# Performance work log

Hardware: AMD Instinct MI355X
Metric: run time of the kernel (lower is better)

## Reference

```python
import jax, jax.numpy as jnp
import numpy as np

N_HEAD = 12
MIN_SIZE = 4
MAX_SIZE = 8
TOP_M = 16
ALPHA = 1.0
EPS = 1e-6
NEG_INF = -1e30


def setup_inputs() -> dict:
    key = jax.random.key(0)
    ks = jax.random.split(key, 4)
    B, T, C = 2, 512, 768
    x = jax.random.normal(ks[0], (B, T, C), jnp.float32)
    w_qkv = jax.random.normal(ks[1], (C, 3 * C), jnp.float32) * (1.0 / np.sqrt(C))
    b_qkv = jnp.zeros((3 * C,), jnp.float32)
    w_proj = jax.random.normal(ks[2], (C, C), jnp.float32) * (1.0 / np.sqrt(C))
    b_proj = jnp.zeros((C,), jnp.float32)
    gate_param = jnp.zeros((), jnp.float32)  # dpp_gate_init = 0.0 -> gate = 0.5
    return {"x": x, "w_qkv": w_qkv, "b_qkv": b_qkv, "w_proj": w_proj,
            "b_proj": b_proj, "gate_param": gate_param}


def _dpp_token(i, q_i, k, v):
    """Greedy DPP subset selection + attention for one query token.
    q_i: [hd], k/v: [T, hd]. Faithful to the torch greedy loop, vectorized
    over candidates with incremental Gram construction (scores only gate the
    discrete selection, so they are computed under stop_gradient, matching
    torch where they only feed Python comparisons)."""
    T, hd = k.shape
    kc = jax.lax.stop_gradient(k)
    qc = jax.lax.stop_gradient(q_i)
    # causal similarity, topk candidates
    sim = jnp.where(jnp.arange(T) <= i, kc @ qc, NEG_INF)
    _, topidx = jax.lax.top_k(sim, TOP_M)  # [M]
    # candidates = top-min(TOP_M, i+1) causal neighbors, excluding i itself
    cand_active = (jnp.arange(TOP_M) < jnp.minimum(TOP_M, i + 1)) & (topidx != i)
    cand_keys = kc[topidx]                              # [M, hd]
    cnorm = jnp.sum(cand_keys * cand_keys, axis=-1)     # [M]

    sel_idx = jnp.zeros((MAX_SIZE,), jnp.int32).at[0].set(i)
    sel_count = jnp.int32(1)
    # initial score: log(det([k_i.k_i]) + eps) / 1**alpha
    cur = jnp.log(jnp.dot(kc[i], kc[i]) + EPS)
    stopped = jnp.bool_(False)
    eye = jnp.eye(MAX_SIZE, dtype=jnp.float32)
    slots = jnp.arange(MAX_SIZE)

    for _ in range(MAX_SIZE - 1):
        rowmask = slots < sel_count                       # [S] current subset rows
        pos = (slots == sel_count).astype(jnp.float32)    # slot for new candidate
        Ksel = kc[sel_idx] * rowmask[:, None].astype(jnp.float32)  # [S, hd]
        G0 = Ksel @ Ksel.T                                # [S, S]
        cross = cand_keys @ Ksel.T                        # [M, S]
        # Gc[c,a,b] = G0[a,b] + pos[a]*cross[c,b] + pos[b]*cross[c,a] + pos[a]pos[b]*cnorm[c]
        Gc = (G0[None]
              + pos[None, :, None] * cross[:, None, :]
              + pos[None, None, :] * cross[:, :, None]
              + (pos[:, None] * pos[None, :])[None] * cnorm[:, None, None])
        newmask = rowmask | (slots == sel_count)
        # identity-pad unused rows/cols so det equals det of the active submatrix
        Gc = Gc + (eye * (1.0 - newmask.astype(jnp.float32)))[None]
        dets = jnp.linalg.det(Gc)                         # [M] (float32, as torch)
        size = (sel_count + 1).astype(jnp.float32)
        score = jnp.log(dets + EPS) / size ** ALPHA       # minimize_det=False
        masked = jnp.where(cand_active, score, NEG_INF)
        best = jnp.argmax(masked)
        best_score = masked[best]
        any_cand = jnp.any(cand_active)
        take = any_cand & (~stopped) & ((best_score > cur) | (sel_count < MIN_SIZE))
        sel_idx = jnp.where(take, sel_idx.at[sel_count].set(topidx[best].astype(jnp.int32)), sel_idx)
        cand_active = jnp.where(take, cand_active.at[best].set(False), cand_active)
        cur = jnp.where(take, best_score, cur)
        sel_count = sel_count + take.astype(jnp.int32)
        stopped = stopped | (~take)

    # attention over the selected subset (gradients flow through k, v, q here)
    rowmask = slots < sel_count
    Ks = k[sel_idx]
    Vs = v[sel_idx]
    logits = jnp.where(rowmask, (Ks @ q_i) / np.float32(np.sqrt(hd)), NEG_INF)
    w = jax.nn.softmax(logits)
    return w @ Vs


def _forward(x, w_qkv, b_qkv, w_proj, b_proj, gate_param):
    B, T, C = x.shape
    hd = C // N_HEAD
    qkv = x @ w_qkv + b_qkv
    q, k, v = jnp.split(qkv, 3, axis=-1)

    def heads(t):  # [B,T,C] -> [B*NH, T, hd]
        return t.reshape(B, T, N_HEAD, hd).transpose(0, 2, 1, 3).reshape(B * N_HEAD, T, hd)

    q, k, v = heads(q), heads(k), heads(v)

    # standard causal softmax attention (flash path, dropout=0 at eval)
    scale = np.float32(1.0 / np.sqrt(hd))
    att = jnp.einsum('nqd,nkd->nqk', q, k) * scale
    causal = jnp.tril(jnp.ones((T, T), bool))
    att = jnp.where(causal[None], att, NEG_INF)
    y_std = jnp.einsum('nqk,nkd->nqd', jax.nn.softmax(att, axis=-1), v)

    # DPP greedy-selection attention, vmapped over tokens and (batch*head)
    dpp_head = jax.vmap(_dpp_token, in_axes=(0, 0, None, None))
    y_dpp = jax.vmap(lambda qh, kh, vh: dpp_head(jnp.arange(T), qh, kh, vh))(q, k, v)

    gate = jax.nn.sigmoid(gate_param)
    y = gate * y_dpp + (1.0 - gate) * y_std
    y = y.reshape(B, N_HEAD, T, hd).transpose(0, 2, 1, 3).reshape(B, T, C)
    return y @ w_proj + b_proj


def reference(x, w_qkv, b_qkv, w_proj, b_proj, gate_param):
    return _forward(x, w_qkv, b_qkv, w_proj, b_proj, gate_param)
```

## Files before the change

### kernel.cpp

```cpp
#include <hip/hip_runtime.h>
#include <math.h>

constexpr int SEQ   = 512;
constexpr int HDIM  = 64;
constexpr int NHEAD = 12;
constexpr int NBATCH = 2;
constexpr int CDIM  = 768;
constexpr int TOPM  = 16;
constexpr int SMAX  = 8;
constexpr float NEGINF = -1e30f;

typedef short bf16x8 __attribute__((ext_vector_type(8)));
typedef float f32x4  __attribute__((ext_vector_type(4)));

__device__ inline void gload_lds16(const void* src, void* lds_base)
{
    __builtin_amdgcn_global_load_lds(
        (const __attribute__((address_space(1))) void*)src,
        (__attribute__((address_space(3))) void*)lds_base, 16, 0, 0);
}

__device__ inline unsigned short f2bf(float f)
{
    unsigned u = __float_as_uint(f);
    return (unsigned short)((u + 0x7FFFu + ((u >> 16) & 1u)) >> 16);
}
__device__ inline float bf2f(unsigned short h)
{
    return __uint_as_float((unsigned)h << 16);
}

__global__ __launch_bounds__(256) void split_x_kernel(
    const float* __restrict__ x, unsigned short* __restrict__ xh,
    unsigned short* __restrict__ xm, unsigned short* __restrict__ xl)
{
    const int idx = (blockIdx.x * 256 + threadIdx.x) * 4;
    float4 v = *(const float4*)(x + idx);
    float vv[4] = {v.x, v.y, v.z, v.w};
    unsigned short h[4], m[4], l[4];
    #pragma unroll
    for (int e = 0; e < 4; ++e) {
        float f = vv[e];
        unsigned short bh = f2bf(f);
        float r1 = f - bf2f(bh);
        unsigned short bm2 = f2bf(r1);
        float r2 = r1 - bf2f(bm2);
        h[e] = bh; m[e] = bm2; l[e] = f2bf(r2);
    }
    *(ushort4*)(xh + idx) = make_ushort4(h[0], h[1], h[2], h[3]);
    *(ushort4*)(xm + idx) = make_ushort4(m[0], m[1], m[2], m[3]);
    *(ushort4*)(xl + idx) = make_ushort4(l[0], l[1], l[2], l[3]);
}

__global__ __launch_bounds__(256) void tsplit_w_kernel(
    const float* __restrict__ w, unsigned short* __restrict__ wh,
    unsigned short* __restrict__ wm, unsigned short* __restrict__ wl)
{
    __shared__ float T[64][65];
    const int c0 = blockIdx.x * 64;
    const int k0 = blockIdx.y * 64;
    const int tid = threadIdx.x;
    #pragma unroll
    for (int i = 0; i < 16; ++i) {
        int idx = tid + i * 256;
        int kk = idx >> 6, cc = idx & 63;
        T[kk][cc] = w[(size_t)(k0 + kk) * (3 * CDIM) + c0 + cc];
    }
    __syncthreads();
    #pragma unroll
    for (int i = 0; i < 16; ++i) {
        int idx = tid + i * 256;
        int col = idx >> 6, kk = idx & 63;
        float f = T[kk][col];
        unsigned short bh = f2bf(f);
        float r1 = f - bf2f(bh);
        unsigned short bm2 = f2bf(r1);
        float r2 = r1 - bf2f(bm2);
        size_t o = (size_t)(c0 + col) * CDIM + k0 + kk;
        wh[o] = bh; wm[o] = bm2; wl[o] = f2bf(r2);
    }
}

__global__ __launch_bounds__(64) void qkv_mfma_kernel(
    const unsigned short* __restrict__ xh, const unsigned short* __restrict__ xm,
    const unsigned short* __restrict__ xl, const unsigned short* __restrict__ wh,
    const unsigned short* __restrict__ wm, const unsigned short* __restrict__ wl,
    const float* __restrict__ bias,
    float* __restrict__ q, float* __restrict__ k, float* __restrict__ v)
{
    __shared__ unsigned short As[3][64 * 32];
    __shared__ unsigned short Bs[3][64 * 32];
    const int bn = blockIdx.x * 64;
    const int bm = blockIdx.y * 64;
    const int tid = threadIdx.x;
    const int lrow = tid & 15;
    const int lk8 = (tid >> 4) << 3;

    f32x4 acc[4][4];
    #pragma unroll
    for (int a = 0; a < 4; ++a)
        #pragma unroll
        for (int b = 0; b < 4; ++b)
            acc[a][b] = (f32x4){0.f, 0.f, 0.f, 0.f};

    const unsigned short* xs[3] = {xh, xm, xl};
    const unsigned short* wsrc[3] = {wh, wm, wl};

    for (int k0 = 0; k0 < CDIM; k0 += 32) {
        #pragma unroll
        for (int c = 0; c < 3; ++c) {
            #pragma unroll
            for (int l = 0; l < 4; ++l) {
                int slot = l * 64 + tid;
                int row = slot >> 2;
                int k8 = (slot & 3) << 3;
                gload_lds16(xs[c] + (size_t)(bm + row) * CDIM + k0 + k8,
                            &As[c][l * 512]);
            }
        }
        #pragma unroll
        for (int c = 0; c < 3; ++c) {
            #pragma unroll
            for (int l = 0; l < 4; ++l) {
                int slot = l * 64 + tid;
                int col = slot >> 2;
                int k8 = (slot & 3) << 3;
                gload_lds16(wsrc[c] + (size_t)(bn + col) * CDIM + k0 + k8,
                            &Bs[c][l * 512]);
            }
        }
        __syncthreads();

        bf16x8 bf[3][4];
        #pragma unroll
        for (int c = 0; c < 3; ++c)
            #pragma unroll
            for (int ni = 0; ni < 4; ++ni)
                bf[c][ni] = *(const bf16x8*)&Bs[c][(ni * 16 + lrow) * 32 + lk8];

        #pragma unroll
        for (int mi = 0; mi < 4; ++mi) {
            bf16x8 ah = *(const bf16x8*)&As[0][(mi * 16 + lrow) * 32 + lk8];
            bf16x8 am = *(const bf16x8*)&As[1][(mi * 16 + lrow) * 32 + lk8];
            bf16x8 al = *(const bf16x8*)&As[2][(mi * 16 + lrow) * 32 + lk8];
            #pragma unroll
            for (int ni = 0; ni < 4; ++ni) {
                f32x4 a = acc[mi][ni];
                a = __builtin_amdgcn_mfma_f32_16x16x32_bf16(al, bf[0][ni], a, 0, 0, 0);
                a = __builtin_amdgcn_mfma_f32_16x16x32_bf16(ah, bf[2][ni], a, 0, 0, 0);
                a = __builtin_amdgcn_mfma_f32_16x16x32_bf16(am, bf[1][ni], a, 0, 0, 0);
                a = __builtin_amdgcn_mfma_f32_16x16x32_bf16(am, bf[0][ni], a, 0, 0, 0);
                a = __builtin_amdgcn_mfma_f32_16x16x32_bf16(ah, bf[1][ni], a, 0, 0, 0);
                a = __builtin_amdgcn_mfma_f32_16x16x32_bf16(ah, bf[0][ni], a, 0, 0, 0);
                acc[mi][ni] = a;
            }
        }
        __syncthreads();
    }

    const int rbase = (tid >> 4) << 2;
    #pragma unroll
    for (int mi = 0; mi < 4; ++mi) {
        #pragma unroll
        for (int ni = 0; ni < 4; ++ni) {
            int cc = bn + ni * 16 + lrow;
            float bval = bias[cc];
            int part = cc / CDIM;
            int c2 = cc - part * CDIM;
            int hh = c2 >> 6, d = c2 & 63;
            float* dst = (part == 0) ? q : ((part == 1) ? k : v);
            #pragma unroll
            for (int r = 0; r < 4; ++r) {
                int m = bm + mi * 16 + rbase + r;
                int b_ = m >> 9, t = m & 511;
                dst[((((size_t)b_ * NHEAD + hh) * SEQ) + t) * HDIM + d] =
                    acc[mi][ni][r] + bval;
            }
        }
    }
}

__global__ __launch_bounds__(256) void qkkt_kernel(
    const float* __restrict__ q, const float* __restrict__ k,
    float* __restrict__ S, float* __restrict__ KKT)
{
    __shared__ float Qs[64][68];
    __shared__ float Ka[64][68];
    __shared__ float Kb[64][68];
    const int e = blockIdx.x;
    const int n = blockIdx.y;
    int it = 0, start = 0;
    while (start + it + 1 <= e) { start += it + 1; ++it; }
    const int jt = e - start;
    const int tid = threadIdx.x;
    const float* qh = q + (size_t)n * SEQ * HDIM;
    const float* kh = k + (size_t)n * SEQ * HDIM;

    #pragma unroll
    for (int l = 0; l < 4; ++l) {
        int idx = tid + l * 256;
        int tok = idx >> 4, d4 = (idx & 15) << 2;
        *(float4*)&Qs[tok][d4] = *(const float4*)(qh + (it * 64 + tok) * HDIM + d4);
        *(float4*)&Ka[tok][d4] = *(const float4*)(kh + (it * 64 + tok) * HDIM + d4);
        *(float4*)&Kb[tok][d4] = *(const float4*)(kh + (jt * 64 + tok) * HDIM + d4);
    }
    __syncthreads();

    const int tm = (tid >> 4) << 2;
    const int tn = (tid & 15) << 2;
    float sacc[4][4] = {};
    float gacc[4][4] = {};
    #pragma unroll 4
    for (int d4 = 0; d4 < 16; ++d4) {
        float4 qr[4], ar[4], br[4];
        #pragma unroll
        for (int u = 0; u < 4; ++u) {
            qr[u] = *(const float4*)&Qs[tm + u][d4 << 2];
            ar[u] = *(const float4*)&Ka[tm + u][d4 << 2];
        }
        #pragma unroll
        for (int w2 = 0; w2 < 4; ++w2)
            br[w2] = *(const float4*)&Kb[tn + w2][d4 << 2];
        #pragma unroll
        for (int u = 0; u < 4; ++u)
            #pragma unroll
            for (int w2 = 0; w2 < 4; ++w2) {
                float s = sacc[u][w2];
                s = fmaf(qr[u].x, br[w2].x, s);
                s = fmaf(qr[u].y, br[w2].y, s);
                s = fmaf(qr[u].z, br[w2].z, s);
                s = fmaf(qr[u].w, br[w2].w, s);
                sacc[u][w2] = s;
                float g = gacc[u][w2];
                g = fmaf(ar[u].x, br[w2].x, g);
                g = fmaf(ar[u].y, br[w2].y, g);
                g = fmaf(ar[u].z, br[w2].z, g);
                g = fmaf(ar[u].w, br[w2].w, g);
                gacc[u][w2] = g;
            }
    }
    float* gdst = KKT + ((size_t)n * 36 + e) * 4096;
    #pragma unroll
    for (int u = 0; u < 4; ++u) {
        int i = it * 64 + tm + u;
        float4 o = {sacc[u][0], sacc[u][1], sacc[u][2], sacc[u][3]};
        *(float4*)(S + ((size_t)n * SEQ + i) * SEQ + jt * 64 + tn) = o;
        float4 g = {gacc[u][0], gacc[u][1], gacc[u][2], gacc[u][3]};
        *(float4*)(gdst + (tm + u) * 64 + tn) = g;
    }
}

__device__ inline double hybrid_log(double a)
{
    unsigned long long b = __double_as_longlong(a);
    int e2 = (int)((b >> 52) & 0x7FF) - 1022;
    double m = __longlong_as_double((b & 0x000FFFFFFFFFFFFFULL) |
                                    0x3FE0000000000000ULL);
    return ((double)__log2f((float)m) + (double)e2) * 0.6931471805599453;
}

__device__ inline double rsqrt64(double x)
{
    double r = (double)rsqrtf((float)x);
    r = r * (1.5 - 0.5 * x * r * r);
    return r;
}

#define CSW(a, b)                                                        \
    {                                                                    \
        bool sw = (v##a < v##b) || ((v##a == v##b) && (j##a > j##b));    \
        float tf = sw ? v##b : v##a;                                     \
        float uf = sw ? v##a : v##b;                                     \
        int ti = sw ? j##b : j##a;                                       \
        int ui = sw ? j##a : j##b;                                       \
        v##a = tf; v##b = uf; j##a = ti; j##b = ui;                      \
    }

__global__ __launch_bounds__(128) void dpp_kernel(
    const float* __restrict__ v, float* __restrict__ S,
    const float* __restrict__ KKT, const float* __restrict__ gate_p,
    float* __restrict__ y, float* __restrict__ denomArr)
{
    const int tid  = threadIdx.x;
    const int wid  = tid >> 6;
    const int lane = tid & 63;
    const int i = blockIdx.x * 2 + wid;
    const int n = blockIdx.y;
    const float* vh = v + (size_t)n * SEQ * HDIM;
    const float* KKTh = KKT + (size_t)n * 36 * 4096;
    float* Srow = S + ((size_t)n * SEQ + i) * SEQ;

    __shared__ float prow[2][SEQ];
    __shared__ float gramf[2][17][17];
    __shared__ int   eidx[2][17];
    __shared__ int   selS[2][SMAX];

    float sim8[8];
    #pragma unroll
    for (int m = 0; m < 8; ++m) {
        int j = lane + (m << 6);
        sim8[m] = (j <= i) ? Srow[j] : NEGINF;
    }
    if (lane < SMAX) selS[wid][lane] = i;

    {
        float v0 = sim8[0], v1 = sim8[1], v2 = sim8[2], v3 = sim8[3],
              v4 = sim8[4], v5 = sim8[5], v6 = sim8[6], v7 = sim8[7];
        int j0 = lane, j1 = lane + 64, j2 = lane + 128, j3 = lane + 192,
            j4 = lane + 256, j5 = lane + 320, j6 = lane + 384, j7 = lane + 448;
        CSW(0, 1) CSW(2, 3) CSW(4, 5) CSW(6, 7)
        CSW(0, 2) CSW(1, 3) CSW(4, 6) CSW(5, 7)
        CSW(1, 2) CSW(5, 6)
        CSW(0, 4) CSW(1, 5) CSW(2, 6) CSW(3, 7)
        CSW(2, 4) CSW(3, 5)
        CSW(1, 2) CSW(3, 4) CSW(5, 6)

        if (lane == 0) eidx[wid][0] = i;
        #pragma unroll
        for (int s = 0; s < TOPM; ++s) {
            float rv = v0;
            #pragma unroll
            for (int off = 32; off; off >>= 1)
                rv = fmaxf(rv, __shfl_xor(rv, off));
            unsigned long long tied = __ballot(v0 == rv);
            int ri;
            if (__popcll(tied) == 1) {
                ri = __shfl(j0, (int)__builtin_ctzll(tied));
            } else {
                int cnd = (v0 == rv) ? j0 : 0x7FFFFFFF;
                #pragma unroll
                for (int off = 32; off; off >>= 1)
                    cnd = min(cnd, __shfl_xor(cnd, off));
                ri = cnd;
            }
            if (lane == 0) eidx[wid][1 + s] = ri;
            if (v0 == rv && j0 == ri) {
                v0 = v1; j0 = j1; v1 = v2; j1 = j2; v2 = v3; j2 = j3;
                v3 = v4; j3 = j4; v4 = v5; j4 = j5; v5 = v6; j5 = j6;
                v6 = v7; j6 = j7; v7 = -3e38f; j7 = 1023;
            }
        }
    }

    const float scale = 0.125f;
    float lm = -3e38f;
    #pragma unroll
    for (int m = 0; m < 8; ++m) lm = fmaxf(lm, sim8[m]);
    #pragma unroll
    for (int off = 32; off; off >>= 1) lm = fmaxf(lm, __shfl_xor(lm, off));
    const float mx = lm * scale;
    float sum = 0.f;
    #pragma unroll
    for (int m = 0; m < 8; ++m) {
        float p = expf(sim8[m] * scale - mx);
        int j = lane + (m << 6);
        prow[wid][j] = p;
        Srow[j] = p;
        sum += p;
    }
    #pragma unroll
    for (int off = 32; off; off >>= 1) sum += __shfl_xor(sum, off);
    const float denom = sum;
    asm volatile("s_waitcnt lgkmcnt(0)" ::: "memory");

    for (int e = lane; e < 153; e += 64) {
        int a = (int)((sqrtf(8.f * (float)e + 1.f) - 1.f) * 0.5f);
        int st = (a * (a + 1)) >> 1;
        if (st > e) { --a; st = (a * (a + 1)) >> 1; }
        else if (st + a + 1 <= e) { ++a; st = (a * (a + 1)) >> 1; }
        int b = e - st;
        int ra = eidx[wid][a], rb = eidx[wid][b];
        int row = ra > rb ? ra : rb;
        int col = ra > rb ? rb : ra;
        int itt = row >> 6, jtt = col >> 6;
        int p = ((itt * (itt + 1)) >> 1) + jtt;
        float s = KKTh[((size_t)p * 64 + (row & 63)) * 64 + (col & 63)];
        gramf[wid][a][b] = s;
        gramf[wid][b][a] = s;
    }
    asm volatile("s_waitcnt lgkmcnt(0)" ::: "memory");

    int sc = 1;
    {
        const int c = lane;
        const bool isCand = (c < TOPM);
        const int nvalid = (i + 1 < TOPM) ? (i + 1) : TOPM;
        bool active = isCand && (c < nvalid) && (eidx[wid][1 + c] != i);
        double zc[7];
        #pragma unroll
        for (int t = 0; t < 7; ++t) zc[t] = 0.0;
        double det = (double)gramf[wid][0][0];
        double cur = 0.0;
        double invL00 = rsqrt64(det > 0.0 ? det : 1e-30);
        double dcv = 0.0;
        if (isCand) {
            zc[0] = (double)gramf[wid][1 + c][0] * invL00;
            dcv = (double)gramf[wid][1 + c][1 + c] - zc[0] * zc[0];
        }

        for (int it2 = 0; it2 < SMAX - 1; ++it2) {
            double argc = det * dcv + 1e-6;
            double key = active ? (argc > 0.0 ? argc : 1e300) : -1.0;
            int rc = c;
            #pragma unroll
            for (int off = 1; off <= 8; off <<= 1) {
                double ov = __shfl_xor(key, off);
                int    oc = __shfl_xor(rc, off);
                if (ov > key || (ov == key && oc < rc)) { key = ov; rc = oc; }
            }
            rc = __shfl(rc, 0);
            bool any = (__any(active ? 1 : 0) != 0);
            double dbest = __shfl(dcv, rc);
            bool take;
            if (it2 < 2) {
                take = any;
            } else {
                double argb = det * dbest + 1e-6;
                bool pos = argb > 0.0;
                double score = hybrid_log(pos ? argb : 1.0) / (double)(sc + 1);
                take = any && (it2 < 3 || (pos && score > cur));
                if (take) cur = pos ? score : __builtin_nan("");
            }
            if (!take) break;

            double invLss = rsqrt64(dbest > 1e-30 ? dbest : 1e-30);
            double zb[7];
            #pragma unroll
            for (int t = 0; t < 7; ++t) zb[t] = __shfl(zc[t], rc);
            if (isCand) {
                double crossn = (double)gramf[wid][1 + c][1 + rc];
                double s2 = 0.0;
                #pragma unroll
                for (int t = 0; t < 7; ++t) s2 += zc[t] * zb[t];
                double znew = (crossn - s2) * invLss;
                #pragma unroll
                for (int t = 0; t < 7; ++t) if (t == sc) zc[t] = znew;
                dcv -= znew * znew;
            }
            det = det * dbest;
            if (c == rc) active = false;
            if (lane == 0) selS[wid][sc] = eidx[wid][1 + rc];
            ++sc;
        }
    }

    int selI[SMAX];
    #pragma unroll
    for (int s = 0; s < SMAX; ++s) selI[s] = selS[wid][s];
    float wsum = 0.f;
    #pragma unroll
    for (int s = 0; s < SMAX; ++s) if (s < sc) wsum += prow[wid][selI[s]];
    float yd = 0.f;
    #pragma unroll
    for (int s = 0; s < SMAX; ++s)
        if (s < sc) yd = fmaf(prow[wid][selI[s]], vh[selI[s] * HDIM + lane], yd);
    const float gp = gate_p[0];
    const float gate = 1.f / (1.f + expf(-gp));
    y[((size_t)n * SEQ + i) * HDIM + lane] = gate * yd / wsum;
    if (lane == 0) denomArr[n * SEQ + i] = denom;
}

__global__ __launch_bounds__(256) void pv_gemm_kernel(
    const float* __restrict__ P, const float* __restrict__ v,
    const float* __restrict__ denomArr, const float* __restrict__ gate_p,
    float* __restrict__ y)
{
    __shared__ float Ps[32][36];
    __shared__ float Vs[32][68];
    const int tt = blockIdx.x;
    const int n  = blockIdx.y;
    const int t0 = tt * 32;
    const int tid = threadIdx.x;
    const float* Ph = P + (size_t)n * SEQ * SEQ;
    const float* vh = v + (size_t)n * SEQ * HDIM;
    const int tm = (tid >> 4) << 1;
    const int tn = (tid & 15) << 2;
    float acc[2][4] = {};
    const int jmax = t0 + 32;
    for (int j0 = 0; j0 < jmax; j0 += 32) {
        {
            int tok = tid >> 3, j4 = (tid & 7) << 2;
            *(float4*)&Ps[tok][j4] =
                *(const float4*)(Ph + (t0 + tok) * SEQ + j0 + j4);
        }
        #pragma unroll
        for (int l = 0; l < 2; ++l) {
            int idx = tid + l * 256;
            int j = idx >> 4, d4 = (idx & 15) << 2;
            *(float4*)&Vs[j][d4] = *(const float4*)(vh + (j0 + j) * HDIM + d4);
        }
        __syncthreads();
        #pragma unroll
        for (int j4 = 0; j4 < 8; ++j4) {
            float4 p0r = *(const float4*)&Ps[tm + 0][j4 << 2];
            float4 p1r = *(const float4*)&Ps[tm + 1][j4 << 2];
            float pr[2][4] = {{p0r.x, p0r.y, p0r.z, p0r.w},
                              {p1r.x, p1r.y, p1r.z, p1r.w}};
            #pragma unroll
            for (int l = 0; l < 4; ++l) {
                float4 v4 = *(const float4*)&Vs[(j4 << 2) + l][tn];
                float vv[4] = {v4.x, v4.y, v4.z, v4.w};
                #pragma unroll
                for (int u = 0; u < 2; ++u)
                    #pragma unroll
                    for (int w2 = 0; w2 < 4; ++w2)
                        acc[u][w2] = fmaf(pr[u][l], vv[w2], acc[u][w2]);
            }
        }
        __syncthreads();
    }
    const float gp = gate_p[0];
    const float gate = 1.f / (1.f + expf(-gp));
    #pragma unroll
    for (int u = 0; u < 2; ++u) {
        int i = t0 + tm + u;
        float den = denomArr[n * SEQ + i];
        #pragma unroll
        for (int w2 = 0; w2 < 4; ++w2) {
            int d = tn + w2;
            size_t off = ((size_t)n * SEQ + i) * HDIM + d;
            y[off] += (1.f - gate) * acc[u][w2] / den;
        }
    }
}

__global__ __launch_bounds__(256) void proj_gemm_kernel(
    const float* __restrict__ y, const float* __restrict__ w,
    float* __restrict__ partial)
{
    __shared__ float As[128][36];
    __shared__ float Bs[32][68];
    const int bm = blockIdx.y * 128;
    const int bn = blockIdx.x * 64;
    const int kbase = blockIdx.z * 96;
    const int tid = threadIdx.x;
    const int tm = (tid >> 4) << 3;
    const int tn = (tid & 15) << 2;
    const int blk = tid >> 3;
    const int bln = (tid & 7) << 3;

    float acc[8][4] = {};
    for (int t = 0; t < 3; ++t) {
        const int k0 = kbase + t * 32;
        float4 av[4];
        #pragma unroll
        for (int l = 0; l < 4; ++l) {
            int idx = tid + l * 256;
            int row = bm + (idx >> 3);
            int col = k0 + ((idx & 7) << 2);
            int b_ = row >> 9, tk = row & 511;
            int h = col >> 6, d = col & 63;
            av[l] = *(const float4*)(y + ((((size_t)b_ * NHEAD + h) * SEQ) + tk) * HDIM + d);
        }
        float4 b0 = *(const float4*)(w + (k0 + blk) * CDIM + bn + bln);
        float4 b1 = *(const float4*)(w + (k0 + blk) * CDIM + bn + bln + 4);
        #pragma unroll
        for (int l = 0; l < 4; ++l) {
            int idx = tid + l * 256;
            int row = idx >> 3, kq = (idx & 7) << 2;
            *(float4*)&As[row][kq] = av[l];
        }
        *(float4*)&Bs[blk][bln] = b0;
        *(float4*)&Bs[blk][bln + 4] = b1;
        __syncthreads();
        #pragma unroll
        for (int k4 = 0; k4 < 8; ++k4) {
            float ar[8][4];
            #pragma unroll
            for (int u = 0; u < 8; ++u) {
                float4 a4 = *(const float4*)&As[tm + u][k4 << 2];
                ar[u][0] = a4.x; ar[u][1] = a4.y;
                ar[u][2] = a4.z; ar[u][3] = a4.w;
            }
            #pragma unroll
            for (int j = 0; j < 4; ++j) {
                float4 b4 = *(const float4*)&Bs[(k4 << 2) + j][tn];
                float bb[4] = {b4.x, b4.y, b4.z, b4.w};
                #pragma unroll
                for (int u = 0; u < 8; ++u)
                    #pragma unroll
                    for (int w2 = 0; w2 < 4; ++w2)
                        acc[u][w2] = fmaf(ar[u][j], bb[w2], acc[u][w2]);
            }
        }
        __syncthreads();
    }
    float* dst = partial + (size_t)blockIdx.z * (1024 * 768);
    #pragma unroll
    for (int u = 0; u < 8; ++u) {
        float4 o = {acc[u][0], acc[u][1], acc[u][2], acc[u][3]};
        *(float4*)(dst + (size_t)(bm + tm + u) * 768 + bn + tn) = o;
    }
}

__global__ __launch_bounds__(256) void proj_reduce_kernel(
    const float* __restrict__ partial, const float* __restrict__ bias,
    float* __restrict__ out)
{
    const int idx = blockIdx.x * 256 + threadIdx.x;
    const int m = idx / 192;
    const int cc = (idx - m * 192) << 2;
    const size_t MN = (size_t)1024 * 768;
    float4 s = *(const float4*)(partial + (size_t)m * 768 + cc);
    #pragma unroll
    for (int z = 1; z < 8; ++z) {
        float4 p = *(const float4*)(partial + (size_t)z * MN + (size_t)m * 768 + cc);
        s.x += p.x; s.y += p.y; s.z += p.z; s.w += p.w;
    }
    float4 b4 = *(const float4*)(bias + cc);
    float4 o = {s.x + b4.x, s.y + b4.y, s.z + b4.z, s.w + b4.w};
    *(float4*)(out + (size_t)m * 768 + cc) = o;
}

extern "C" void kernel_launch(void* const* d_in, const int* in_sizes, int n_in,
                              void* d_out, int out_size, void* d_ws, size_t ws_size,
                              hipStream_t stream)
{
    const float* x      = (const float*)d_in[0];
    const float* w_qkv  = (const float*)d_in[1];
    const float* b_qkv  = (const float*)d_in[2];
    const float* w_proj = (const float*)d_in[3];
    const float* b_proj = (const float*)d_in[4];
    const float* gate_p = (const float*)d_in[5];
    float* out = (float*)d_out;

    float* ws = (float*)d_ws;
    const size_t HS = (size_t)NBATCH * NHEAD * SEQ * HDIM;
    const size_t SS = (size_t)NBATCH * NHEAD * SEQ * SEQ;
    float* q   = ws;
    float* k   = q + HS;
    float* v   = k + HS;
    float* y   = v + HS;
    float* S   = y + HS;
    float* den = S + SS;
    float* KKT = den + 16384;

    unsigned short* us = (unsigned short*)S;
    unsigned short* xh = us;
    unsigned short* xm = us + 786432;
    unsigned short* xl = us + 1572864;
    unsigned short* wh = us + 2359296;
    unsigned short* wm = us + 2359296 + 1769472;
    unsigned short* wl = us + 2359296 + 3538944;

    split_x_kernel<<<768, 256, 0, stream>>>(x, xh, xm, xl);
    tsplit_w_kernel<<<dim3(36, 12), 256, 0, stream>>>(w_qkv, wh, wm, wl);
    qkv_mfma_kernel<<<dim3(36, 16), 64, 0, stream>>>(
        xh, xm, xl, wh, wm, wl, b_qkv, q, k, v);
    qkkt_kernel<<<dim3(36, NBATCH * NHEAD), 256, 0, stream>>>(q, k, S, KKT);
    dpp_kernel<<<dim3(SEQ / 2, NBATCH * NHEAD), 128, 0, stream>>>(
        v, S, KKT, gate_p, y, den);
    pv_gemm_kernel<<<dim3(SEQ / 32, NBATCH * NHEAD), 256, 0, stream>>>(
        S, v, den, gate_p, y);
    proj_gemm_kernel<<<dim3(CDIM / 64, (NBATCH * SEQ) / 128, 8), 256, 0, stream>>>(
        y, w_proj, S);
    proj_reduce_kernel<<<768, 256, 0, stream>>>(S, b_proj, out);
}
```

Measured before the change: 177.6 us.

## Move QK/KKT and output projection to split-bf16 MFMA, drop LDS staging

Replaces the FP32 FMA QK^T/K K^T kernel and the split-K projection GEMM plus reduce with 3-way bf16-split MFMA kernels. The QKV epilogue now writes Q and K pre-split into hi/mid/lo bf16 planes. The QKV GEMM drops LDS staging in favour of direct global fragment loads with smaller 32-row tiles and more blocks. This moves the dense matmuls onto matrix cores and removes the partial-sum reduction pass. In exchange it adds extra split kernels, more global traffic from unshared fragment loads, and precision that depends on the 6-product bf16 emulation.

```diff
diff --git a/kernel.cpp b/kernel.cpp
--- a/kernel.cpp
+++ b/kernel.cpp
@@ -13,13 +13,6 @@
 typedef short bf16x8 __attribute__((ext_vector_type(8)));
 typedef float f32x4  __attribute__((ext_vector_type(4)));
 
-__device__ inline void gload_lds16(const void* src, void* lds_base)
-{
-    __builtin_amdgcn_global_load_lds(
-        (const __attribute__((address_space(1))) void*)src,
-        (__attribute__((address_space(3))) void*)lds_base, 16, 0, 0);
-}
-
 __device__ inline unsigned short f2bf(float f)
 {
     unsigned u = __float_as_uint(f);
@@ -28,6 +21,26 @@
 __device__ inline float bf2f(unsigned short h)
 {
     return __uint_as_float((unsigned)h << 16);
+}
+__device__ inline void split3(float f, unsigned short& h,
+                              unsigned short& m, unsigned short& l)
+{
+    h = f2bf(f);
+    float r1 = f - bf2f(h);
+    m = f2bf(r1);
+    l = f2bf(r1 - bf2f(m));
+}
+
+__device__ inline f32x4 mfma6(bf16x8 ah, bf16x8 am, bf16x8 al,
+                              bf16x8 bh, bf16x8 bm, bf16x8 bl, f32x4 a)
+{
+    a = __builtin_amdgcn_mfma_f32_16x16x32_bf16(al, bh, a, 0, 0, 0);
+    a = __builtin_amdgcn_mfma_f32_16x16x32_bf16(ah, bl, a, 0, 0, 0);
+    a = __builtin_amdgcn_mfma_f32_16x16x32_bf16(am, bm, a, 0, 0, 0);
+    a = __builtin_amdgcn_mfma_f32_16x16x32_bf16(am, bh, a, 0, 0, 0);
+    a = __builtin_amdgcn_mfma_f32_16x16x32_bf16(ah, bm, a, 0, 0, 0);
+    a = __builtin_amdgcn_mfma_f32_16x16x32_bf16(ah, bh, a, 0, 0, 0);
+    return a;
 }
 
 __global__ __launch_bounds__(256) void split_x_kernel(
@@ -39,21 +52,14 @@
     float vv[4] = {v.x, v.y, v.z, v.w};
     unsigned short h[4], m[4], l[4];
     #pragma unroll
-    for (int e = 0; e < 4; ++e) {
-        float f = vv[e];
-        unsigned short bh = f2bf(f);
-        float r1 = f - bf2f(bh);
-        unsigned short bm2 = f2bf(r1);
-        float r2 = r1 - bf2f(bm2);
-        h[e] = bh; m[e] = bm2; l[e] = f2bf(r2);
-    }
+    for (int e = 0; e < 4; ++e) split3(vv[e], h[e], m[e], l[e]);
     *(ushort4*)(xh + idx) = make_ushort4(h[0], h[1], h[2], h[3]);
     *(ushort4*)(xm + idx) = make_ushort4(m[0], m[1], m[2], m[3]);
     *(ushort4*)(xl + idx) = make_ushort4(l[0], l[1], l[2], l[3]);
 }
 
-__global__ __launch_bounds__(256) void tsplit_w_kernel(
-    const float* __restrict__ w, unsigned short* __restrict__ wh,
+__global__ __launch_bounds__(256) void tsplit_kernel(
+    const float* __restrict__ w, int ncols, unsigned short* __restrict__ wh,
     unsigned short* __restrict__ wm, unsigned short* __restrict__ wl)
 {
     __shared__ float T[64][65];
@@ -64,21 +70,37 @@
     for (int i = 0; i < 16; ++i) {
         int idx = tid + i * 256;
         int kk = idx >> 6, cc = idx & 63;
-        T[kk][cc] = w[(size_t)(k0 + kk) * (3 * CDIM) + c0 + cc];
+        T[kk][cc] = w[(size_t)(k0 + kk) * ncols + c0 + cc];
     }
     __syncthreads();
     #pragma unroll
     for (int i = 0; i < 16; ++i) {
         int idx = tid + i * 256;
         int col = idx >> 6, kk = idx & 63;
-        float f = T[kk][col];
-        unsigned short bh = f2bf(f);
-        float r1 = f - bf2f(bh);
-        unsigned short bm2 = f2bf(r1);
-        float r2 = r1 - bf2f(bm2);
+        unsigned short h, m, l;
+        split3(T[kk][col], h, m, l);
         size_t o = (size_t)(c0 + col) * CDIM + k0 + kk;
-        wh[o] = bh; wm[o] = bm2; wl[o] = f2bf(r2);
-    }
+        wh[o] = h; wm[o] = m; wl[o] = l;
+    }
+}
+
+__global__ __launch_bounds__(256) void split_y_kernel(
+    const float* __restrict__ y, unsigned short* __restrict__ yh,
+    unsigned short* __restrict__ ym, unsigned short* __restrict__ yl)
+{
+    const int fl = (blockIdx.x * 256 + threadIdx.x) * 4;
+    const int m = fl / CDIM;
+    const int c0 = fl - m * CDIM;
+    const int b_ = m >> 9, t = m & 511;
+    const int hh = c0 >> 6, d = c0 & 63;
+    float4 v = *(const float4*)(y + ((((size_t)b_ * NHEAD + hh) * SEQ) + t) * HDIM + d);
+    float vv[4] = {v.x, v.y, v.z, v.w};
+    unsigned short h[4], mm[4], l[4];
+    #pragma unroll
+    for (int e = 0; e < 4; ++e) split3(vv[e], h[e], mm[e], l[e]);
+    *(ushort4*)(yh + fl) = make_ushort4(h[0], h[1], h[2], h[3]);
+    *(ushort4*)(ym + fl) = make_ushort4(mm[0], mm[1], mm[2], mm[3]);
+    *(ushort4*)(yl + fl) = make_ushort4(l[0], l[1], l[2], l[3]);
 }
 
 __global__ __launch_bounds__(64) void qkv_mfma_kernel(
@@ -86,81 +108,50 @@
     const unsigned short* __restrict__ xl, const unsigned short* __restrict__ wh,
     const unsigned short* __restrict__ wm, const unsigned short* __restrict__ wl,
     const float* __restrict__ bias,
-    float* __restrict__ q, float* __restrict__ k, float* __restrict__ v)
-{
-    __shared__ unsigned short As[3][64 * 32];
-    __shared__ unsigned short Bs[3][64 * 32];
+    unsigned short* __restrict__ qh, unsigned short* __restrict__ qm,
+    unsigned short* __restrict__ ql, unsigned short* __restrict__ kh,
+    unsigned short* __restrict__ km, unsigned short* __restrict__ kl,
+    float* __restrict__ v)
+{
     const int bn = blockIdx.x * 64;
-    const int bm = blockIdx.y * 64;
-    const int tid = threadIdx.x;
-    const int lrow = tid & 15;
-    const int lk8 = (tid >> 4) << 3;
-
-    f32x4 acc[4][4];
-    #pragma unroll
-    for (int a = 0; a < 4; ++a)
-        #pragma unroll
-        for (int b = 0; b < 4; ++b)
-            acc[a][b] = (f32x4){0.f, 0.f, 0.f, 0.f};
-
-    const unsigned short* xs[3] = {xh, xm, xl};
-    const unsigned short* wsrc[3] = {wh, wm, wl};
+    const int bm = blockIdx.y * 32;
+    const int lane = threadIdx.x;
+    const int lrow = lane & 15;
+    const int lk8 = (lane >> 4) << 3;
+
+    f32x4 acc[2][4];
+    #pragma unroll
+    for (int a = 0; a < 2; ++a)
+        #pragma unroll
+        for (int b = 0; b < 4; ++b) acc[a][b] = (f32x4){0.f, 0.f, 0.f, 0.f};
 
     for (int k0 = 0; k0 < CDIM; k0 += 32) {
-        #pragma unroll
-        for (int c = 0; c < 3; ++c) {
-            #pragma unroll
-            for (int l = 0; l < 4; ++l) {
-                int slot = l * 64 + tid;
-                int row = slot >> 2;
-                int k8 = (slot & 3) << 3;
-                gload_lds16(xs[c] + (size_t)(bm + row) * CDIM + k0 + k8,
-                            &As[c][l * 512]);
-            }
-        }
-        #pragma unroll
-        for (int c = 0; c < 3; ++c) {
-            #pragma unroll
-            for (int l = 0; l < 4; ++l) {
-                int slot = l * 64 + tid;
-                int col = slot >> 2;
-                int k8 = (slot & 3) << 3;
-                gload_lds16(wsrc[c] + (size_t)(bn + col) * CDIM + k0 + k8,
-                            &Bs[c][l * 512]);
-            }
-        }
-        __syncthreads();
-
-        bf16x8 bf[3][4];
-        #pragma unroll
-        for (int c = 0; c < 3; ++c)
+        bf16x8 af[3][2], bf[3][4];
+        #pragma unroll
+        for (int mi = 0; mi < 2; ++mi) {
+            size_t ro = (size_t)(bm + mi * 16 + lrow) * CDIM + k0 + lk8;
+            af[0][mi] = *(const bf16x8*)(xh + ro);
+            af[1][mi] = *(const bf16x8*)(xm + ro);
+            af[2][mi] = *(const bf16x8*)(xl + ro);
+        }
+        #pragma unroll
+        for (int ni = 0; ni < 4; ++ni) {
+            size_t ro = (size_t)(bn + ni * 16 + lrow) * CDIM + k0 + lk8;
+            bf[0][ni] = *(const bf16x8*)(wh + ro);
+            bf[1][ni] = *(const bf16x8*)(wm + ro);
+            bf[2][ni] = *(const bf16x8*)(wl + ro);
+        }
+        #pragma unroll
+        for (int mi = 0; mi < 2; ++mi)
             #pragma unroll
             for (int ni = 0; ni < 4; ++ni)
-                bf[c][ni] = *(const bf16x8*)&Bs[c][(ni * 16 + lrow) * 32 + lk8];
-
-        #pragma unroll
-        for (int mi = 0; mi < 4; ++mi) {
-            bf16x8 ah = *(const bf16x8*)&As[0][(mi * 16 + lrow) * 32 + lk8];
-            bf16x8 am = *(const bf16x8*)&As[1][(mi * 16 + lrow) * 32 + lk8];
-            bf16x8 al = *(const bf16x8*)&As[2][(mi * 16 + lrow) * 32 + lk8];
-            #pragma unroll
-            for (int ni = 0; ni < 4; ++ni) {
-                f32x4 a = acc[mi][ni];
-                a = __builtin_amdgcn_mfma_f32_16x16x32_bf16(al, bf[0][ni], a, 0, 0, 0);
-                a = __builtin_amdgcn_mfma_f32_16x16x32_bf16(ah, bf[2][ni], a, 0, 0, 0);
-                a = __builtin_amdgcn_mfma_f32_16x16x32_bf16(am, bf[1][ni], a, 0, 0, 0);
-                a = __builtin_amdgcn_mfma_f32_16x16x32_bf16(am, bf[0][ni], a, 0, 0, 0);
-                a = __builtin_amdgcn_mfma_f32_16x16x32_bf16(ah, bf[1][ni], a, 0, 0, 0);
-                a = __builtin_amdgcn_mfma_f32_16x16x32_bf16(ah, bf[0][ni], a, 0, 0, 0);
-                acc[mi][ni] = a;
-            }
-        }
-        __syncthreads();
-    }
-
-    const int rbase = (tid >> 4) << 2;
-    #pragma unroll
-    for (int mi = 0; mi < 4; ++mi) {
+                acc[mi][ni] = mfma6(af[0][mi], af[1][mi], af[2][mi],
+                                    bf[0][ni], bf[1][ni], bf[2][ni], acc[mi][ni]);
+    }
+
+    const int rbase = (lane >> 4) << 2;
+    #pragma unroll
+    for (int mi = 0; mi < 2; ++mi) {
         #pragma unroll
         for (int ni = 0; ni < 4; ++ni) {
             int cc = bn + ni * 16 + lrow;
@@ -168,85 +159,102 @@
             int part = cc / CDIM;
             int c2 = cc - part * CDIM;
             int hh = c2 >> 6, d = c2 & 63;
-            float* dst = (part == 0) ? q : ((part == 1) ? k : v);
             #pragma unroll
             for (int r = 0; r < 4; ++r) {
                 int m = bm + mi * 16 + rbase + r;
                 int b_ = m >> 9, t = m & 511;
-                dst[((((size_t)b_ * NHEAD + hh) * SEQ) + t) * HDIM + d] =
-                    acc[mi][ni][r] + bval;
-            }
-        }
-    }
-}
-
-__global__ __launch_bounds__(256) void qkkt_kernel(
-    const float* __restrict__ q, const float* __restrict__ k,
+                size_t off = ((((size_t)b_ * NHEAD + hh) * SEQ) + t) * HDIM + d;
+                float val = acc[mi][ni][r] + bval;
+                if (part == 2) {
+                    v[off] = val;
+                } else {
+                    unsigned short h2, m2, l2;
+                    split3(val, h2, m2, l2);
+                    if (part == 0) { qh[off] = h2; qm[off] = m2; ql[off] = l2; }
+                    else           { kh[off] = h2; km[off] = m2; kl[off] = l2; }
+                }
+            }
+        }
+    }
+}
+
+__global__ __launch_bounds__(64) void qkkt_mfma_kernel(
+    const unsigned short* __restrict__ qh, const unsigned short* __restrict__ qm,
+    const unsigned short* __restrict__ ql, const unsigned short* __restrict__ kh,
+    const unsigned short* __restrict__ km, const unsigned short* __restrict__ kl,
     float* __restrict__ S, float* __restrict__ KKT)
 {
-    __shared__ float Qs[64][68];
-    __shared__ float Ka[64][68];
-    __shared__ float Kb[64][68];
     const int e = blockIdx.x;
     const int n = blockIdx.y;
+    const int z = blockIdx.z;
     int it = 0, start = 0;
     while (start + it + 1 <= e) { start += it + 1; ++it; }
     const int jt = e - start;
-    const int tid = threadIdx.x;
-    const float* qh = q + (size_t)n * SEQ * HDIM;
-    const float* kh = k + (size_t)n * SEQ * HDIM;
-
-    #pragma unroll
-    for (int l = 0; l < 4; ++l) {
-        int idx = tid + l * 256;
-        int tok = idx >> 4, d4 = (idx & 15) << 2;
-        *(float4*)&Qs[tok][d4] = *(const float4*)(qh + (it * 64 + tok) * HDIM + d4);
-        *(float4*)&Ka[tok][d4] = *(const float4*)(kh + (it * 64 + tok) * HDIM + d4);
-        *(float4*)&Kb[tok][d4] = *(const float4*)(kh + (jt * 64 + tok) * HDIM + d4);
-    }
-    __syncthreads();
-
-    const int tm = (tid >> 4) << 2;
-    const int tn = (tid & 15) << 2;
-    float sacc[4][4] = {};
-    float gacc[4][4] = {};
-    #pragma unroll 4
-    for (int d4 = 0; d4 < 16; ++d4) {
-        float4 qr[4], ar[4], br[4];
-        #pragma unroll
-        for (int u = 0; u < 4; ++u) {
-            qr[u] = *(const float4*)&Qs[tm + u][d4 << 2];
-            ar[u] = *(const float4*)&Ka[tm + u][d4 << 2];
-        }
-        #pragma unroll
-        for (int w2 = 0; w2 < 4; ++w2)
-            br[w2] = *(const float4*)&Kb[tn + w2][d4 << 2];
-        #pragma unroll
-        for (int u = 0; u < 4; ++u)
-            #pragma unroll
-            for (int w2 = 0; w2 < 4; ++w2) {
-                float s = sacc[u][w2];
-                s = fmaf(qr[u].x, br[w2].x, s);
-                s = fmaf(qr[u].y, br[w2].y, s);
-                s = fmaf(qr[u].z, br[w2].z, s);
-                s = fmaf(qr[u].w, br[w2].w, s);
-                sacc[u][w2] = s;
-                float g = gacc[u][w2];
-                g = fmaf(ar[u].x, br[w2].x, g);
-                g = fmaf(ar[u].y, br[w2].y, g);
-                g = fmaf(ar[u].z, br[w2].z, g);
-                g = fmaf(ar[u].w, br[w2].w, g);
-                gacc[u][w2] = g;
-            }
-    }
-    float* gdst = KKT + ((size_t)n * 36 + e) * 4096;
-    #pragma unroll
-    for (int u = 0; u < 4; ++u) {
-        int i = it * 64 + tm + u;
-        float4 o = {sacc[u][0], sacc[u][1], sacc[u][2], sacc[u][3]};
-        *(float4*)(S + ((size_t)n * SEQ + i) * SEQ + jt * 64 + tn) = o;
-        float4 g = {gacc[u][0], gacc[u][1], gacc[u][2], gacc[u][3]};
-        *(float4*)(gdst + (tm + u) * 64 + tn) = g;
+    const int lane = threadIdx.x;
+    const int lrow = lane & 15;
+    const int lk8 = (lane >> 4) << 3;
+    const size_t base = (size_t)n * SEQ * HDIM;
+
+    const unsigned short* A0 = z ? kh : qh;
+    const unsigned short* A1 = z ? km : qm;
+    const unsigned short* A2 = z ? kl : ql;
+
+    f32x4 acc[4][4];
+    #pragma unroll
+    for (int a = 0; a < 4; ++a)
+        #pragma unroll
+        for (int b = 0; b < 4; ++b) acc[a][b] = (f32x4){0.f, 0.f, 0.f, 0.f};
+
+    #pragma unroll
+    for (int ks = 0; ks < 2; ++ks) {
+        const int k0 = ks * 32;
+        bf16x8 af[3][4], bf[3][4];
+        #pragma unroll
+        for (int mi = 0; mi < 4; ++mi) {
+            size_t ro = base + (size_t)(it * 64 + mi * 16 + lrow) * HDIM + k0 + lk8;
+            af[0][mi] = *(const bf16x8*)(A0 + ro);
+            af[1][mi] = *(const bf16x8*)(A1 + ro);
+            af[2][mi] = *(const bf16x8*)(A2 + ro);
+        }
+        #pragma unroll
+        for (int ni = 0; ni < 4; ++ni) {
+            size_t ro = base + (size_t)(jt * 64 + ni * 16 + lrow) * HDIM + k0 + lk8;
+            bf[0][ni] = *(const bf16x8*)(kh + ro);
+            bf[1][ni] = *(const bf16x8*)(km + ro);
+            bf[2][ni] = *(const bf16x8*)(kl + ro);
+        }
+        #pragma unroll
+        for (int mi = 0; mi < 4; ++mi)
+            #pragma unroll
+            for (int ni = 0; ni < 4; ++ni)
+                acc[mi][ni] = mfma6(af[0][mi], af[1][mi], af[2][mi],
+                                    bf[0][ni], bf[1][ni], bf[2][ni], acc[mi][ni]);
+    }
+
+    const int rbase = (lane >> 4) << 2;
+    if (z == 0) {
+        #pragma unroll
+        for (int mi = 0; mi < 4; ++mi)
+            #pragma unroll
+            for (int ni = 0; ni < 4; ++ni) {
+                int col = jt * 64 + ni * 16 + lrow;
+                #pragma unroll
+                for (int r = 0; r < 4; ++r) {
+                    int row = it * 64 + mi * 16 + rbase + r;
+                    S[((size_t)n * SEQ + row) * SEQ + col] = acc[mi][ni][r];
+                }
+            }
+    } else {
+        float* gdst = KKT + ((size_t)n * 36 + e) * 4096;
+        #pragma unroll
+        for (int mi = 0; mi < 4; ++mi)
+            #pragma unroll
+            for (int ni = 0; ni < 4; ++ni) {
+                int col = ni * 16 + lrow;
+                #pragma unroll
+                for (int r = 0; r < 4; ++r)
+                    gdst[(mi * 16 + rbase + r) * 64 + col] = acc[mi][ni][r];
+            }
     }
 }
 
@@ -524,92 +532,61 @@
     }
 }
 
-__global__ __launch_bounds__(256) void proj_gemm_kernel(
-    const float* __restrict__ y, const float* __restrict__ w,
-    float* __restrict__ partial)
-{
-    __shared__ float As[128][36];
-    __shared__ float Bs[32][68];
-    const int bm = blockIdx.y * 128;
+__global__ __launch_bounds__(64) void proj_mfma_kernel(
+    const unsigned short* __restrict__ ah, const unsigned short* __restrict__ am,
+    const unsigned short* __restrict__ al, const unsigned short* __restrict__ bh,
+    const unsigned short* __restrict__ bm2, const unsigned short* __restrict__ bl,
+    const float* __restrict__ bias, float* __restrict__ out)
+{
     const int bn = blockIdx.x * 64;
-    const int kbase = blockIdx.z * 96;
-    const int tid = threadIdx.x;
-    const int tm = (tid >> 4) << 3;
-    const int tn = (tid & 15) << 2;
-    const int blk = tid >> 3;
-    const int bln = (tid & 7) << 3;
-
-    float acc[8][4] = {};
-    for (int t = 0; t < 3; ++t) {
-        const int k0 = kbase + t * 32;
-        float4 av[4];
-        #pragma unroll
-        for (int l = 0; l < 4; ++l) {
-            int idx = tid + l * 256;
-            int row = bm + (idx >> 3);
-            int col = k0 + ((idx & 7) << 2);
-            int b_ = row >> 9, tk = row & 511;
-            int h = col >> 6, d = col & 63;
-            av[l] = *(const float4*)(y + ((((size_t)b_ * NHEAD + h) * SEQ) + tk) * HDIM + d);
-        }
-        float4 b0 = *(const float4*)(w + (k0 + blk) * CDIM + bn + bln);
-        float4 b1 = *(const float4*)(w + (k0 + blk) * CDIM + bn + bln + 4);
-        #pragma unroll
-        for (int l = 0; l < 4; ++l) {
-            int idx = tid + l * 256;
-            int row = idx >> 3, kq = (idx & 7) << 2;
-            *(float4*)&As[row][kq] = av[l];
-        }
-        *(float4*)&Bs[blk][bln] = b0;
-        *(float4*)&Bs[blk][bln + 4] = b1;
-        __syncthreads();
-        #pragma unroll
-        for (int k4 = 0; k4 < 8; ++k4) {
-            float ar[8][4];
-            #pragma unroll
-            for (int u = 0; u < 8; ++u) {
-                float4 a4 = *(const float4*)&As[tm + u][k4 << 2];
-                ar[u][0] = a4.x; ar[u][1] = a4.y;
-                ar[u][2] = a4.z; ar[u][3] = a4.w;
-            }
-            #pragma unroll
-            for (int j = 0; j < 4; ++j) {
-                float4 b4 = *(const float4*)&Bs[(k4 << 2) + j][tn];
-                float bb[4] = {b4.x, b4.y, b4.z, b4.w};
-                #pragma unroll
-                for (int u = 0; u < 8; ++u)
-                    #pragma unroll
-                    for (int w2 = 0; w2 < 4; ++w2)
-                        acc[u][w2] = fmaf(ar[u][j], bb[w2], acc[u][w2]);
-            }
-        }
-        __syncthreads();
-    }
-    float* dst = partial + (size_t)blockIdx.z * (1024 * 768);
-    #pragma unroll
-    for (int u = 0; u < 8; ++u) {
-        float4 o = {acc[u][0], acc[u][1], acc[u][2], acc[u][3]};
-        *(float4*)(dst + (size_t)(bm + tm + u) * 768 + bn + tn) = o;
-    }
-}
-
-__global__ __launch_bounds__(256) void proj_reduce_kernel(
-    const float* __restrict__ partial, const float* __restrict__ bias,
-    float* __restrict__ out)
-{
-    const int idx = blockIdx.x * 256 + threadIdx.x;
-    const int m = idx / 192;
-    const int cc = (idx - m * 192) << 2;
-    const size_t MN = (size_t)1024 * 768;
-    float4 s = *(const float4*)(partial + (size_t)m * 768 + cc);
-    #pragma unroll
-    for (int z = 1; z < 8; ++z) {
-        float4 p = *(const float4*)(partial + (size_t)z * MN + (size_t)m * 768 + cc);
-        s.x += p.x; s.y += p.y; s.z += p.z; s.w += p.w;
-    }
-    float4 b4 = *(const float4*)(bias + cc);
-    float4 o = {s.x + b4.x, s.y + b4.y, s.z + b4.z, s.w + b4.w};
-    *(float4*)(out + (size_t)m * 768 + cc) = o;
+    const int bmr = blockIdx.y * 32;
+    const int lane = threadIdx.x;
+    const int lrow = lane & 15;
+    const int lk8 = (lane >> 4) << 3;
+
+    f32x4 acc[2][4];
+    #pragma unroll
+    for (int a = 0; a < 2; ++a)
+        #pragma unroll
+        for (int b = 0; b < 4; ++b) acc[a][b] = (f32x4){0.f, 0.f, 0.f, 0.f};
+
+    for (int k0 = 0; k0 < CDIM; k0 += 32) {
+        bf16x8 af[3][2], bf[3][4];
+        #pragma unroll
+        for (int mi = 0; mi < 2; ++mi) {
+            size_t ro = (size_t)(bmr + mi * 16 + lrow) * CDIM + k0 + lk8;
+            af[0][mi] = *(const bf16x8*)(ah + ro);
+            af[1][mi] = *(const bf16x8*)(am + ro);
+            af[2][mi] = *(const bf16x8*)(al + ro);
+        }
+        #pragma unroll
+        for (int ni = 0; ni < 4; ++ni) {
+            size_t ro = (size_t)(bn + ni * 16 + lrow) * CDIM + k0 + lk8;
+            bf[0][ni] = *(const bf16x8*)(bh + ro);
+            bf[1][ni] = *(const bf16x8*)(bm2 + ro);
+            bf[2][ni] = *(const bf16x8*)(bl + ro);
+        }
+        #pragma unroll
+        for (int mi = 0; mi < 2; ++mi)
+            #pragma unroll
+            for (int ni = 0; ni < 4; ++ni)
+                acc[mi][ni] = mfma6(af[0][mi], af[1][mi], af[2][mi],
+                                    bf[0][ni], bf[1][ni], bf[2][ni], acc[mi][ni]);
+    }
+
+    const int rbase = (lane >> 4) << 2;
+    #pragma unroll
+    for (int mi = 0; mi < 2; ++mi)
+        #pragma unroll
+        for (int ni = 0; ni < 4; ++ni) {
+            int cc = bn + ni * 16 + lrow;
+            float bval = bias[cc];
+            #pragma unroll
+            for (int r = 0; r < 4; ++r) {
+                int m = bmr + mi * 16 + rbase + r;
+                out[(size_t)m * CDIM + cc] = acc[mi][ni][r] + bval;
+            }
+        }
 }
 
 extern "C" void kernel_launch(void* const* d_in, const int* in_sizes, int n_in,
@@ -627,32 +604,47 @@
     float* ws = (float*)d_ws;
     const size_t HS = (size_t)NBATCH * NHEAD * SEQ * HDIM;
     const size_t SS = (size_t)NBATCH * NHEAD * SEQ * SEQ;
-    float* q   = ws;
-    float* k   = q + HS;
-    float* v   = k + HS;
-    float* y   = v + HS;
-    float* S   = y + HS;
+
+    unsigned short* cb = (unsigned short*)ws;
+    unsigned short* qh = cb;
+    unsigned short* qm = cb + HS;
+    unsigned short* ql = cb + 2 * HS;
+    unsigned short* kh = cb + 3 * HS;
+    unsigned short* km = cb + 4 * HS;
+    unsigned short* kl = cb + 5 * HS;
+    float* y   = ws + 2 * HS;
+    float* v   = ws + 3 * HS;
+    float* S   = ws + 4 * HS;
     float* den = S + SS;
     float* KKT = den + 16384;
 
     unsigned short* us = (unsigned short*)S;
     unsigned short* xh = us;
-    unsigned short* xm = us + 786432;
-    unsigned short* xl = us + 1572864;
-    unsigned short* wh = us + 2359296;
-    unsigned short* wm = us + 2359296 + 1769472;
-    unsigned short* wl = us + 2359296 + 3538944;
+    unsigned short* xm = us + HS;
+    unsigned short* xl = us + 2 * HS;
+    unsigned short* wqh = us + 3 * HS;
+    unsigned short* wqm = us + 3 * HS + 1769472;
+    unsigned short* wql = us + 3 * HS + 2 * 1769472;
+
+    unsigned short* yh = us;
+    unsigned short* ym = us + HS;
+    unsigned short* yl = us + 2 * HS;
+    unsigned short* wph = us + 3 * HS;
+    unsigned short* wpm = us + 3 * HS + 589824;
+    unsigned short* wpl = us + 3 * HS + 2 * 589824;
 
     split_x_kernel<<<768, 256, 0, stream>>>(x, xh, xm, xl);
-    tsplit_w_kernel<<<dim3(36, 12), 256, 0, stream>>>(w_qkv, wh, wm, wl);
-    qkv_mfma_kernel<<<dim3(36, 16), 64, 0, stream>>>(
-        xh, xm, xl, wh, wm, wl, b_qkv, q, k, v);
-    qkkt_kernel<<<dim3(36, NBATCH * NHEAD), 256, 0, stream>>>(q, k, S, KKT);
+    tsplit_kernel<<<dim3(36, 12), 256, 0, stream>>>(w_qkv, 3 * CDIM, wqh, wqm, wql);
+    qkv_mfma_kernel<<<dim3(36, 32), 64, 0, stream>>>(
+        xh, xm, xl, wqh, wqm, wql, b_qkv, qh, qm, ql, kh, km, kl, v);
+    qkkt_mfma_kernel<<<dim3(36, NBATCH * NHEAD, 2), 64, 0, stream>>>(
+        qh, qm, ql, kh, km, kl, S, KKT);
     dpp_kernel<<<dim3(SEQ / 2, NBATCH * NHEAD), 128, 0, stream>>>(
         v, S, KKT, gate_p, y, den);
     pv_gemm_kernel<<<dim3(SEQ / 32, NBATCH * NHEAD), 256, 0, stream>>>(
         S, v, den, gate_p, y);
-    proj_gemm_kernel<<<dim3(CDIM / 64, (NBATCH * SEQ) / 128, 8), 256, 0, stream>>>(
-        y, w_proj, S);
-    proj_reduce_kernel<<<768, 256, 0, stream>>>(S, b_proj, out);
-}
+    split_y_kernel<<<768, 256, 0, stream>>>(y, yh, ym, yl);
+    tsplit_kernel<<<dim3(12, 12), 256, 0, stream>>>(w_proj, CDIM, wph, wpm, wpl);
+    proj_mfma_kernel<<<dim3(12, 32), 64, 0, stream>>>(
+        yh, ym, yl, wph, wpm, wpl, b_proj, out);
+}
```

Measured after the change: 215.9 us. 21.6% more time.
